# Optimization experiments

Measured on AMD Instinct MI355X. Metric: run time of the kernel, lower is better.

Reference implementation:

```python
import jax, jax.numpy as jnp
import numpy as np

M, N, D = 4096, 50, 100
HID = 512
T_FINAL, S0 = 1.0, 0.0
R = 0.05      # rate in phi(t,X,Y,Z) = R*(Y - sum(X*Z))
SIG = 0.4     # sigma(t,X,Y) = SIG * diag(X)


def _xavier(key, fan_in, fan_out):
    lim = float(np.sqrt(6.0 / (fan_in + fan_out)))
    return jax.random.uniform(key, (fan_in, fan_out), jnp.float32, -lim, lim)


def setup_inputs() -> dict:
    key = jax.random.key(0)
    k_dw, k_xi, k0, k1, k2, k3, k4 = jax.random.split(key, 7)
    dt = (T_FINAL - S0) / N
    # fetch_minibatch(): Dt[:,0]=s, Dt[:,1:]=dt; DW[:,1:]=sqrt(dt)*normal; then cumsum
    Dt = jnp.concatenate([jnp.full((M, 1, 1), S0, jnp.float32),
                          jnp.full((M, N, 1), dt, jnp.float32)], axis=1)
    DW = jnp.concatenate([jnp.zeros((M, 1, D), jnp.float32),
                          jnp.sqrt(dt) * jax.random.normal(k_dw, (M, N, D), jnp.float32)], axis=1)
    t = jnp.cumsum(Dt, axis=1)   # (M, N+1, 1)
    W = jnp.cumsum(DW, axis=1)   # (M, N+1, D)
    Xi = jnp.where(jnp.arange(D) % 2 == 0, 1.0, 0.5)[None, :].astype(jnp.float32)  # (1, D)
    sizes = [D + 1, HID, HID, HID, HID, 1]
    keys = [k0, k1, k2, k3, k4]
    inp = {"t": t, "W": W, "Xi": Xi}
    for i in range(5):
        inp[f"Wm{i}"] = _xavier(keys[i], sizes[i], sizes[i + 1])
        inp[f"b{i}"] = jnp.zeros((sizes[i + 1],), jnp.float32)
    return inp


def _mlp(params, tX):
    # neural_net.forward: sin activations on hidden layers, linear out
    h = tX
    for Wl, bl in params[:-1]:
        h = jnp.sin(h @ Wl + bl)
    Wl, bl = params[-1]
    return h @ Wl + bl  # (M, 1)


def _net_u_Du(params, t, X):
    # u = fn_u([t, X]); Du = d(sum u)/dX via VJP with ones cotangent
    u, vjp = jax.vjp(lambda X_: _mlp(params, jnp.concatenate([t, X_], axis=1)), X)
    (Du,) = vjp(jnp.ones_like(u))
    return u, Du


def _loss(t, W, Xi, params):
    t0, W0 = t[:, 0, :], W[:, 0, :]
    X0 = jnp.tile(Xi, (M, 1))
    Y0, Z0 = _net_u_Du(params, t0, X0)

    def step(carry, inp):
        t0, W0, X0, Y0, Z0, acc = carry
        t1, W1 = inp                                   # (M,1), (M,D)
        dt = t1 - t0
        dW = W1 - W0
        s_dW = SIG * X0 * dW                           # diag(SIG*X0) @ dW, elementwise
        phi = R * (Y0 - jnp.sum(X0 * Z0, axis=1, keepdims=True))
        Y1_tilde = Y0 + phi * dt + jnp.sum(Z0 * s_dW, axis=1, keepdims=True)
        X1 = X0 + s_dW                                 # mu = 0 (Black-Scholes-Barenblatt)
        Y1, Z1 = _net_u_Du(params, t1, X1)
        acc = acc + jnp.sum((Y1 - Y1_tilde) ** 2)
        return (t1, W1, X1, Y1, Z1, acc), None

    ts = jnp.moveaxis(t[:, 1:, :], 1, 0)  # (N, M, 1)
    Ws = jnp.moveaxis(W[:, 1:, :], 1, 0)  # (N, M, D)
    (tN, WN, XN, YN, ZN, sum0N), _ = jax.lax.scan(
        step, (t0, W0, X0, Y0, Z0, jnp.float32(0.0)), (ts, Ws))
    gX = jnp.sum(XN ** 2, axis=1, keepdims=True)       # g(X) = |X|^2
    loss_uT = jnp.sum((YN - gX) ** 2)
    loss_DuT = jnp.sum((ZN - 2.0 * XN) ** 2)
    return (sum0N + loss_uT + loss_DuT) / M            # loss_n == 1 (default)


def reference(t, W, Xi, Wm0, b0, Wm1, b1, Wm2, b2, Wm3, b3, Wm4, b4):
    params = [(Wm0, b0), (Wm1, b1), (Wm2, b2), (Wm3, b3), (Wm4, b4)]
    return _loss(t, W, Xi, params)
```

## Files before the change

kernel.cpp:

```cpp
#include <hip/hip_runtime.h>
#include <cstdint>
#include <cstddef>

#define MM 4096
#define NSTEP 50
#define DD 100
#define HID 512
#define K0P 128
#define SIGC 0.4f
#define RC 0.05f
#define BMR 16
#define NWG (MM / BMR)
#define GSC 16.0f

typedef long fp8x8;
typedef float f32x4 __attribute__((ext_vector_type(4)));
union Pack4 { __bf16 h[4]; uint2 u2; };

typedef const __attribute__((address_space(1))) void* gvp;
typedef __attribute__((address_space(3))) void* lvp;
static __device__ __forceinline__ void load_lds16(const void* g, void* l) {
    __builtin_amdgcn_global_load_lds((gvp)g, (lvp)l, 16, 0, 0);
}

template <int N>
static __device__ __forceinline__ void wait_vmcnt() {
    if constexpr (N == 0)      asm volatile("s_waitcnt vmcnt(0)" ::: "memory");
    else if constexpr (N == 1) asm volatile("s_waitcnt vmcnt(1)" ::: "memory");
    else if constexpr (N == 2) asm volatile("s_waitcnt vmcnt(2)" ::: "memory");
    else if constexpr (N == 4) asm volatile("s_waitcnt vmcnt(4)" ::: "memory");
    __builtin_amdgcn_sched_barrier(0);
}

static __device__ __forceinline__ unsigned char to_fp8(float x) {
    return (unsigned char)(__builtin_amdgcn_cvt_pk_fp8_f32(x, 0.f, 0, false) & 0xff);
}
static __device__ __forceinline__ unsigned pack4_fp8(float a, float b, float c, float d) {
    int w = __builtin_amdgcn_cvt_pk_fp8_f32(a, b, 0, false);
    w = __builtin_amdgcn_cvt_pk_fp8_f32(c, d, w, true);
    return (unsigned)w;
}

__global__ void k_transpose(const float* __restrict__ in, unsigned char* __restrict__ out,
                            int Ksrc, int Kpad, int N) {
    int idx = blockIdx.x * 256 + threadIdx.x;
    if (idx >= N * Kpad) return;
    int n = idx / Kpad, k = idx - n * Kpad;
    out[idx] = (k < Ksrc) ? to_fp8(in[k * N + n]) : (unsigned char)0;
}

__global__ void k_cast(const float* __restrict__ in, unsigned char* __restrict__ out,
                       int Rsrc, int Rpad, int C) {
    int idx = blockIdx.x * 256 + threadIdx.x;
    if (idx >= Rpad * C) return;
    int r = idx / C;
    out[idx] = (r < Rsrc) ? to_fp8(in[idx]) : (unsigned char)0;
}

__global__ __launch_bounds__(256) void k_init(const float* __restrict__ t,
                                              const float* __restrict__ Xi,
                                              float* __restrict__ X0,
                                              unsigned char* __restrict__ tXg) {
    int m = blockIdx.x * 4 + (threadIdx.x >> 6);
    int lane = threadIdx.x & 63;
    for (int ii = 0; ii < 2; ii++) {
        int d = lane + ii * 64;
        if (d < DD) {
            float x = Xi[d];
            X0[m * DD + d] = x;
            tXg[(size_t)m * K0P + 1 + d] = to_fp8(x);
        } else if (d < K0P - 1) {
            tXg[(size_t)m * K0P + 1 + d] = 0;
        }
    }
    if (lane == 0) tXg[(size_t)m * K0P] = to_fp8(t[m * (NSTEP + 1)]);
}

template <int K, int NBLK, int NJB, int ASTR, int EPI>
__device__ __forceinline__ void phaseP(
    int tid, const unsigned char* __restrict__ Bw,
    const char* __restrict__ Rin, char* __restrict__ Rout, char* __restrict__ Bb,
    const float* __restrict__ bias, const float* __restrict__ W4,
    Pack4 (&stash)[2][2], float* __restrict__ u_lds) {

    constexpr int NKB = K / 64;
    constexpr int NJ  = NBLK / 128;
    constexpr int CB  = NBLK * 64;
    constexpr int SB  = CB / 8;
    constexpr int I   = SB / 1024;
    constexpr int NQ  = NJB * NKB;

    const int wave = tid >> 6, lane = tid & 63;
    const int lr = lane & 15, lg = lane >> 4;
    const int am = lr;
    const int wrow0 = wave * (NBLK / 8);

    int bRow[I], bG[I];
    #pragma unroll
    for (int it = 0; it < I; it++) {
        int c16 = it * 64 + lane;
        bRow[it] = c16 >> 2;
        bG[it]   = (c16 & 3) ^ ((bRow[it] >> 1) & 3);
    }

    #define STG(q)                                                              \
        {   char* dst_ = Bb + ((q) % 3) * CB + wave * SB;                       \
            _Pragma("unroll")                                                   \
            for (int it = 0; it < I; it++)                                      \
                load_lds16(Bw + (size_t)(((q) / NKB) * NBLK + wrow0 + bRow[it]) * K \
                               + ((q) % NKB) * 64 + bG[it] * 16,                \
                           dst_ + it * 1024); }

    STG(0)
    if (NQ > 1) STG(1)

    float up = 0.f;
    f32x4 acc[NJ];
    #pragma unroll
    for (int q = 0; q < NQ; q++) {
        const int jb = q / NKB, kb = q % NKB;
        if (kb == 0) {
            #pragma unroll
            for (int nj = 0; nj < NJ; nj++) acc[nj] = f32x4{0.f, 0.f, 0.f, 0.f};
        }
        if (q + 1 < NQ) wait_vmcnt<I>(); else wait_vmcnt<0>();
        if (q + 2 < NQ) STG(q + 2)
        const char* slot = Bb + (q % 3) * CB + wave * SB;
        #pragma unroll
        for (int ks = 0; ks < 2; ks++) {
            int kcA = kb * 8 + ks * 4 + lg;
            fp8x8 aF = *(const fp8x8*)(Rin + am * ASTR +
                        ((((kcA >> 1) ^ (am & 7))) << 4) + (kcA & 1) * 8);
            int kcB = ks * 4 + lg;
            #pragma unroll
            for (int nj = 0; nj < NJ; nj++) {
                int rl = nj * 16 + lr;
                fp8x8 bF = *(const fp8x8*)(slot + rl * 64 +
                            ((((kcB >> 1) ^ ((rl >> 1) & 3))) << 4) + (kcB & 1) * 8);
                acc[nj] = __builtin_amdgcn_mfma_f32_16x16x32_fp8_fp8(
                    bF, aF, acc[nj], 0, 0, 0);
            }
        }
        if (kb == NKB - 1) {
            #pragma unroll
            for (int nj = 0; nj < NJ; nj++) {
                const int n0 = jb * NBLK + wrow0 + nj * 16 + lg * 4;
                if (EPI == 3) {
                    f32x4 z = acc[nj];
                    z *= (1.0f / GSC);
                    *(f32x4*)((float*)Rout + am * 132 + n0) = z;
                } else {
                    const int po = am * 512 + (((n0 >> 4) ^ (am & 7)) << 4) +
                                   ((n0 >> 3) & 1) * 8 + (n0 & 7);
                    if (EPI == 0) {
                        f32x4 bv = *(const f32x4*)(bias + n0);
                        float s[4], c[4];
                        #pragma unroll
                        for (int r = 0; r < 4; r++)
                            __sincosf(acc[nj][r] + bv[r], &s[r], &c[r]);
                        *(unsigned*)(Rout + po) = pack4_fp8(s[0], s[1], s[2], s[3]);
                        Pack4 pc;
                        #pragma unroll
                        for (int r = 0; r < 4; r++) pc.h[r] = (__bf16)c[r];
                        stash[jb][nj] = pc;
                    } else if (EPI == 1) {
                        f32x4 bv = *(const f32x4*)(bias + n0);
                        f32x4 wv = *(const f32x4*)(W4 + n0);
                        float g[4];
                        #pragma unroll
                        for (int r = 0; r < 4; r++) {
                            float s, c;
                            __sincosf(acc[nj][r] + bv[r], &s, &c);
                            up += s * wv[r];
                            g[r] = c * wv[r] * GSC;
                        }
                        *(unsigned*)(Rout + po) = pack4_fp8(g[0], g[1], g[2], g[3]);
                    } else {
                        Pack4 pm = stash[jb][nj];
                        *(unsigned*)(Rout + po) = pack4_fp8(
                            acc[nj][0] * (float)pm.h[0], acc[nj][1] * (float)pm.h[1],
                            acc[nj][2] * (float)pm.h[2], acc[nj][3] * (float)pm.h[3]);
                    }
                }
            }
        }
    }
    #undef STG

    if (EPI == 1) {
        up += __shfl_xor(up, 16);
        up += __shfl_xor(up, 32);
        if (lg == 0) atomicAdd(&u_lds[am], up);
    }
}

__global__ __launch_bounds__(512, 1) void mega(
    const float* __restrict__ t, const float* __restrict__ W,
    const unsigned char* __restrict__ wt0, const unsigned char* __restrict__ wt1,
    const unsigned char* __restrict__ wt2, const unsigned char* __restrict__ wt3,
    const unsigned char* __restrict__ wd0, const unsigned char* __restrict__ wd1,
    const unsigned char* __restrict__ wd2, const unsigned char* __restrict__ wd3,
    const float* __restrict__ b0, const float* __restrict__ b1,
    const float* __restrict__ b2, const float* __restrict__ b3,
    const float* __restrict__ W4, const float* __restrict__ b4,
    unsigned char* __restrict__ tXg, float* __restrict__ X,
    float* __restrict__ Ytil, float* __restrict__ accG, int n) {

    extern __shared__ char lds[];
    char*  tXL   = lds;
    char*  R0    = lds + 2048;
    char*  R1    = lds + 10240;
    float* Zf    = (float*)(lds + 18432);
    char*  Bb    = lds + 27648;
    float* u_lds = (float*)(lds + 76800);

    const int tid = threadIdx.x;
    const int wgrow = blockIdx.x * BMR;
    const int em = tid >> 5, edg = tid & 31, ed0 = edg * 4;
    const int grow = wgrow + em;
    const int lane = tid & 63, wave = tid >> 6;
    const float b4v = b4[0];

    Pack4 st0[2][2], st1[2][2], st2[2][2];

    if (tid < 128) {
        int m = tid >> 3, pc = tid & 7;
        load_lds16(tXg + (size_t)(wgrow + m) * K0P + ((pc ^ (m & 7)) << 4),
                   tXL + wave * 1024 + lane * 16);
    }
    __syncthreads();

    phaseP<128, 256, 2, 128, 0>(tid, wt0, tXL, R0, Bb, b0, nullptr, st0, u_lds);
    __syncthreads();
    phaseP<512, 256, 2, 512, 0>(tid, wt1, R0, R1, Bb, b1, nullptr, st1, u_lds);
    __syncthreads();
    phaseP<512, 256, 2, 512, 0>(tid, wt2, R1, R0, Bb, b2, nullptr, st2, u_lds);
    __syncthreads();
    if (tid < BMR) u_lds[tid] = 0.f;
    __syncthreads();
    phaseP<512, 256, 2, 512, 1>(tid, wt3, R0, R1, Bb, b3, W4, st0 , u_lds);
    __syncthreads();
    phaseP<512, 256, 2, 512, 2>(tid, wd3, R1, R0, Bb, nullptr, nullptr, st2, u_lds);
    __syncthreads();
    phaseP<512, 256, 2, 512, 2>(tid, wd2, R0, R1, Bb, nullptr, nullptr, st1, u_lds);
    __syncthreads();
    phaseP<512, 256, 2, 512, 2>(tid, wd1, R1, R0, Bb, nullptr, nullptr, st0, u_lds);
    __syncthreads();
    phaseP<512, 128, 1, 512, 3>(tid, wd0, R0, (char*)Zf, Bb, nullptr, nullptr, st0, u_lds);
    __syncthreads();

    float u_reg = u_lds[em] + b4v;
    float resid_l = 0.f;
    if (n >= 1 && edg == 0) {
        float dd = u_reg - Ytil[grow];
        resid_l = dd * dd;
    }
    const float* Zs = Zf + em * 132;
    if (n < NSTEP) {
        float t0v = t[grow * (NSTEP + 1) + n];
        float t1v = t[grow * (NSTEP + 1) + n + 1];
        const float* Wr = W + ((size_t)grow * (NSTEP + 1) + n) * DD;
        float pXZ = 0.f, pZs = 0.f;
        #pragma unroll
        for (int i = 0; i < 4; i++) {
            int d = ed0 + i;
            if (d < DD) {
                float x0 = X[grow * DD + d];
                float z = Zs[1 + d];
                float dWv = Wr[DD + d] - Wr[d];
                float s = SIGC * x0 * dWv;
                pXZ += x0 * z;
                pZs += z * s;
                float x1 = x0 + s;
                X[grow * DD + d] = x1;
                tXg[(size_t)grow * K0P + 1 + d] = to_fp8(x1);
            }
        }
        pXZ += __shfl_xor(pXZ, 1); pXZ += __shfl_xor(pXZ, 2);
        pXZ += __shfl_xor(pXZ, 4); pXZ += __shfl_xor(pXZ, 8);
        pXZ += __shfl_xor(pXZ, 16);
        pZs += __shfl_xor(pZs, 1); pZs += __shfl_xor(pZs, 2);
        pZs += __shfl_xor(pZs, 4); pZs += __shfl_xor(pZs, 8);
        pZs += __shfl_xor(pZs, 16);
        if (edg == 0) {
            float phi = RC * (u_reg - pXZ);
            Ytil[grow] = u_reg + phi * (t1v - t0v) + pZs;
            tXg[(size_t)grow * K0P] = to_fp8(t1v);
        }
    } else {
        float gX = 0.f, sD = 0.f;
        #pragma unroll
        for (int i = 0; i < 4; i++) {
            int d = ed0 + i;
            if (d < DD) {
                float x0 = X[grow * DD + d];
                float z = Zs[1 + d];
                gX += x0 * x0;
                float e = z - 2.f * x0;
                sD += e * e;
            }
        }
        gX += __shfl_xor(gX, 1); gX += __shfl_xor(gX, 2);
        gX += __shfl_xor(gX, 4); gX += __shfl_xor(gX, 8);
        gX += __shfl_xor(gX, 16);
        sD += __shfl_xor(sD, 1); sD += __shfl_xor(sD, 2);
        sD += __shfl_xor(sD, 4); sD += __shfl_xor(sD, 8);
        sD += __shfl_xor(sD, 16);
        if (edg == 0) {
            float e = u_reg - gX;
            resid_l += e * e + sD;
        }
    }

    float r = resid_l;
    r += __shfl_xor(r, 32);
    r += __shfl_xor(r, 16);
    r += __shfl_xor(r, 8);
    r += __shfl_xor(r, 4);
    r += __shfl_xor(r, 2);
    r += __shfl_xor(r, 1);
    float* red = u_lds + 16;
    if (lane == 0) red[wave] = r;
    __syncthreads();
    if (tid == 0) {
        float s = 0.f;
        #pragma unroll
        for (int i = 0; i < 8; i++) s += red[i];
        atomicAdd(accG, s);
    }
}

__global__ void k_final(const float* __restrict__ acc, float* __restrict__ out) {
    out[0] = acc[0] / (float)MM;
}

extern "C" void kernel_launch(void* const* d_in, const int* in_sizes, int n_in,
                              void* d_out, int out_size, void* d_ws, size_t ws_size,
                              hipStream_t stream) {
    (void)in_sizes; (void)n_in; (void)out_size; (void)ws_size;
    const float* t  = (const float*)d_in[0];
    const float* W  = (const float*)d_in[1];
    const float* Xi = (const float*)d_in[2];
    const float* Wm[5];
    const float* bb[5];
    for (int i = 0; i < 5; i++) {
        Wm[i] = (const float*)d_in[3 + 2 * i];
        bb[i] = (const float*)d_in[4 + 2 * i];
    }

    char* p = (char*)d_ws;
    auto alloc = [&](size_t bytes) -> void* {
        void* r = (void*)p;
        p += (bytes + 255) & ~(size_t)255;
        return r;
    };

    unsigned char* wt[4];
    wt[0] = (unsigned char*)alloc((size_t)HID * K0P);
    for (int i = 1; i < 4; i++) wt[i] = (unsigned char*)alloc((size_t)HID * HID);
    unsigned char* wd[4];
    wd[0] = (unsigned char*)alloc((size_t)K0P * HID);
    for (int i = 1; i < 4; i++) wd[i] = (unsigned char*)alloc((size_t)HID * HID);
    unsigned char* tXg = (unsigned char*)alloc((size_t)MM * K0P);
    float* X    = (float*)alloc((size_t)MM * DD * 4);
    float* Ytil = (float*)alloc((size_t)MM * 4);
    float* acc  = (float*)alloc(256);

    hipMemsetAsync(acc, 0, 256, stream);

    k_transpose<<<(HID * K0P + 255) / 256, 256, 0, stream>>>(Wm[0], wt[0], 101, K0P, HID);
    for (int i = 1; i < 4; i++)
        k_transpose<<<(HID * HID + 255) / 256, 256, 0, stream>>>(Wm[i], wt[i], HID, HID, HID);
    k_cast<<<(K0P * HID + 255) / 256, 256, 0, stream>>>(Wm[0], wd[0], 101, K0P, HID);
    for (int i = 1; i < 4; i++)
        k_cast<<<(HID * HID + 255) / 256, 256, 0, stream>>>(Wm[i], wd[i], HID, HID, HID);

    k_init<<<MM / 4, 256, 0, stream>>>(t, Xi, X, tXg);

    const int LDSB = 77056;
    hipFuncSetAttribute((const void*)mega,
                        hipFuncAttributeMaxDynamicSharedMemorySize, LDSB);

    for (int n = 0; n <= NSTEP; n++) {
        mega<<<dim3(NWG), dim3(512), LDSB, stream>>>(
            t, W,
            wt[0], wt[1], wt[2], wt[3],
            wd[0], wd[1], wd[2], wd[3],
            bb[0], bb[1], bb[2], bb[3],
            Wm[4], bb[4],
            tXg, X, Ytil, acc, n);
    }

    k_final<<<1, 1, 0, stream>>>(acc, (float*)d_out);
}
```

Baseline: 1.469 ms.

## Fuse three timesteps per kernel launch and widen GEMM N-block to 512

The mega kernel now runs SPAN=3 consecutive timesteps in one launch. X and Ytil stay in registers across those steps, and the fp8 network input is rewritten directly into LDS instead of being reloaded from global memory each step. This cuts the launch count about threefold and removes per-step global round-trips for X and the input tile. The GEMM phases also drop the two-pass N loop: each wave now covers 512 output columns with four accumulators, which roughly doubles the B staging buffers to about 125 KB of LDS and adds register pressure.

```diff
diff --git a/kernel.cpp b/kernel.cpp
--- a/kernel.cpp
+++ b/kernel.cpp
@@ -12,6 +12,7 @@
 #define BMR 16
 #define NWG (MM / BMR)
 #define GSC 16.0f
+#define SPAN 3
 
 typedef long fp8x8;
 typedef float f32x4 __attribute__((ext_vector_type(4)));
@@ -76,19 +77,18 @@
     if (lane == 0) tXg[(size_t)m * K0P] = to_fp8(t[m * (NSTEP + 1)]);
 }
 
-template <int K, int NBLK, int NJB, int ASTR, int EPI>
+template <int K, int NBLK, int ASTR, int EPI>
 __device__ __forceinline__ void phaseP(
     int tid, const unsigned char* __restrict__ Bw,
     const char* __restrict__ Rin, char* __restrict__ Rout, char* __restrict__ Bb,
     const float* __restrict__ bias, const float* __restrict__ W4,
-    Pack4 (&stash)[2][2], float* __restrict__ u_lds) {
-
-    constexpr int NKB = K / 64;
+    Pack4 (&stash)[4], float* __restrict__ u_lds) {
+
+    constexpr int NQ  = K / 64;
     constexpr int NJ  = NBLK / 128;
     constexpr int CB  = NBLK * 64;
     constexpr int SB  = CB / 8;
     constexpr int I   = SB / 1024;
-    constexpr int NQ  = NJB * NKB;
 
     const int wave = tid >> 6, lane = tid & 63;
     const int lr = lane & 15, lg = lane >> 4;
@@ -107,28 +107,23 @@
         {   char* dst_ = Bb + ((q) % 3) * CB + wave * SB;                       \
             _Pragma("unroll")                                                   \
             for (int it = 0; it < I; it++)                                      \
-                load_lds16(Bw + (size_t)(((q) / NKB) * NBLK + wrow0 + bRow[it]) * K \
-                               + ((q) % NKB) * 64 + bG[it] * 16,                \
+                load_lds16(Bw + (size_t)(wrow0 + bRow[it]) * K                  \
+                               + (q) * 64 + bG[it] * 16,                        \
                            dst_ + it * 1024); }
 
     STG(0)
     if (NQ > 1) STG(1)
 
     float up = 0.f;
-    f32x4 acc[NJ];
+    f32x4 acc[NJ] = {};
     #pragma unroll
     for (int q = 0; q < NQ; q++) {
-        const int jb = q / NKB, kb = q % NKB;
-        if (kb == 0) {
-            #pragma unroll
-            for (int nj = 0; nj < NJ; nj++) acc[nj] = f32x4{0.f, 0.f, 0.f, 0.f};
-        }
         if (q + 1 < NQ) wait_vmcnt<I>(); else wait_vmcnt<0>();
         if (q + 2 < NQ) STG(q + 2)
         const char* slot = Bb + (q % 3) * CB + wave * SB;
         #pragma unroll
         for (int ks = 0; ks < 2; ks++) {
-            int kcA = kb * 8 + ks * 4 + lg;
+            int kcA = q * 8 + ks * 4 + lg;
             fp8x8 aF = *(const fp8x8*)(Rin + am * ASTR +
                         ((((kcA >> 1) ^ (am & 7))) << 4) + (kcA & 1) * 8);
             int kcB = ks * 4 + lg;
@@ -141,51 +136,50 @@
                     bF, aF, acc[nj], 0, 0, 0);
             }
         }
-        if (kb == NKB - 1) {
-            #pragma unroll
-            for (int nj = 0; nj < NJ; nj++) {
-                const int n0 = jb * NBLK + wrow0 + nj * 16 + lg * 4;
-                if (EPI == 3) {
-                    f32x4 z = acc[nj];
-                    z *= (1.0f / GSC);
-                    *(f32x4*)((float*)Rout + am * 132 + n0) = z;
-                } else {
-                    const int po = am * 512 + (((n0 >> 4) ^ (am & 7)) << 4) +
-                                   ((n0 >> 3) & 1) * 8 + (n0 & 7);
-                    if (EPI == 0) {
-                        f32x4 bv = *(const f32x4*)(bias + n0);
-                        float s[4], c[4];
-                        #pragma unroll
-                        for (int r = 0; r < 4; r++)
-                            __sincosf(acc[nj][r] + bv[r], &s[r], &c[r]);
-                        *(unsigned*)(Rout + po) = pack4_fp8(s[0], s[1], s[2], s[3]);
-                        Pack4 pc;
-                        #pragma unroll
-                        for (int r = 0; r < 4; r++) pc.h[r] = (__bf16)c[r];
-                        stash[jb][nj] = pc;
-                    } else if (EPI == 1) {
-                        f32x4 bv = *(const f32x4*)(bias + n0);
-                        f32x4 wv = *(const f32x4*)(W4 + n0);
-                        float g[4];
-                        #pragma unroll
-                        for (int r = 0; r < 4; r++) {
-                            float s, c;
-                            __sincosf(acc[nj][r] + bv[r], &s, &c);
-                            up += s * wv[r];
-                            g[r] = c * wv[r] * GSC;
-                        }
-                        *(unsigned*)(Rout + po) = pack4_fp8(g[0], g[1], g[2], g[3]);
-                    } else {
-                        Pack4 pm = stash[jb][nj];
-                        *(unsigned*)(Rout + po) = pack4_fp8(
-                            acc[nj][0] * (float)pm.h[0], acc[nj][1] * (float)pm.h[1],
-                            acc[nj][2] * (float)pm.h[2], acc[nj][3] * (float)pm.h[3]);
-                    }
+    }
+    #undef STG
+
+    #pragma unroll
+    for (int nj = 0; nj < NJ; nj++) {
+        const int n0 = wrow0 + nj * 16 + lg * 4;
+        if (EPI == 3) {
+            f32x4 z = acc[nj];
+            z *= (1.0f / GSC);
+            *(f32x4*)((float*)Rout + am * 132 + n0) = z;
+        } else {
+            const int po = am * 512 + (((n0 >> 4) ^ (am & 7)) << 4) +
+                           ((n0 >> 3) & 1) * 8 + (n0 & 7);
+            if (EPI == 0) {
+                f32x4 bv = *(const f32x4*)(bias + n0);
+                float s[4], c[4];
+                #pragma unroll
+                for (int r = 0; r < 4; r++)
+                    __sincosf(acc[nj][r] + bv[r], &s[r], &c[r]);
+                *(unsigned*)(Rout + po) = pack4_fp8(s[0], s[1], s[2], s[3]);
+                Pack4 pc;
+                #pragma unroll
+                for (int r = 0; r < 4; r++) pc.h[r] = (__bf16)c[r];
+                stash[nj] = pc;
+            } else if (EPI == 1) {
+                f32x4 bv = *(const f32x4*)(bias + n0);
+                f32x4 wv = *(const f32x4*)(W4 + n0);
+                float g[4];
+                #pragma unroll
+                for (int r = 0; r < 4; r++) {
+                    float s, c;
+                    __sincosf(acc[nj][r] + bv[r], &s, &c);
+                    up += s * wv[r];
+                    g[r] = c * wv[r] * GSC;
                 }
+                *(unsigned*)(Rout + po) = pack4_fp8(g[0], g[1], g[2], g[3]);
+            } else {
+                Pack4 pm = stash[nj];
+                *(unsigned*)(Rout + po) = pack4_fp8(
+                    acc[nj][0] * (float)pm.h[0], acc[nj][1] * (float)pm.h[1],
+                    acc[nj][2] * (float)pm.h[2], acc[nj][3] * (float)pm.h[3]);
             }
         }
     }
-    #undef STG
 
     if (EPI == 1) {
         up += __shfl_xor(up, 16);
@@ -204,15 +198,15 @@
     const float* __restrict__ b2, const float* __restrict__ b3,
     const float* __restrict__ W4, const float* __restrict__ b4,
     unsigned char* __restrict__ tXg, float* __restrict__ X,
-    float* __restrict__ Ytil, float* __restrict__ accG, int n) {
+    float* __restrict__ Ytil, float* __restrict__ accG, int n0) {
 
     extern __shared__ char lds[];
     char*  tXL   = lds;
     char*  R0    = lds + 2048;
     char*  R1    = lds + 10240;
     float* Zf    = (float*)(lds + 18432);
-    char*  Bb    = lds + 27648;
-    float* u_lds = (float*)(lds + 76800);
+    char*  Bb    = lds + 26880;
+    float* u_lds = (float*)(lds + 125184);
 
     const int tid = threadIdx.x;
     const int wgrow = blockIdx.x * BMR;
@@ -221,7 +215,16 @@
     const int lane = tid & 63, wave = tid >> 6;
     const float b4v = b4[0];
 
-    Pack4 st0[2][2], st1[2][2], st2[2][2];
+    Pack4 st0[4], st1[4], st2[4];
+
+    float x[4];
+    #pragma unroll
+    for (int i = 0; i < 4; i++) {
+        int d = ed0 + i;
+        x[i] = (d < DD) ? X[grow * DD + d] : 0.f;
+    }
+    float ytil = Ytil[grow];
+    float resid_l = 0.f;
 
     if (tid < 128) {
         int m = tid >> 3, pc = tid & 7;
@@ -230,87 +233,100 @@
     }
     __syncthreads();
 
-    phaseP<128, 256, 2, 128, 0>(tid, wt0, tXL, R0, Bb, b0, nullptr, st0, u_lds);
-    __syncthreads();
-    phaseP<512, 256, 2, 512, 0>(tid, wt1, R0, R1, Bb, b1, nullptr, st1, u_lds);
-    __syncthreads();
-    phaseP<512, 256, 2, 512, 0>(tid, wt2, R1, R0, Bb, b2, nullptr, st2, u_lds);
-    __syncthreads();
-    if (tid < BMR) u_lds[tid] = 0.f;
-    __syncthreads();
-    phaseP<512, 256, 2, 512, 1>(tid, wt3, R0, R1, Bb, b3, W4, st0 , u_lds);
-    __syncthreads();
-    phaseP<512, 256, 2, 512, 2>(tid, wd3, R1, R0, Bb, nullptr, nullptr, st2, u_lds);
-    __syncthreads();
-    phaseP<512, 256, 2, 512, 2>(tid, wd2, R0, R1, Bb, nullptr, nullptr, st1, u_lds);
-    __syncthreads();
-    phaseP<512, 256, 2, 512, 2>(tid, wd1, R1, R0, Bb, nullptr, nullptr, st0, u_lds);
-    __syncthreads();
-    phaseP<512, 128, 1, 512, 3>(tid, wd0, R0, (char*)Zf, Bb, nullptr, nullptr, st0, u_lds);
-    __syncthreads();
-
-    float u_reg = u_lds[em] + b4v;
-    float resid_l = 0.f;
-    if (n >= 1 && edg == 0) {
-        float dd = u_reg - Ytil[grow];
-        resid_l = dd * dd;
-    }
-    const float* Zs = Zf + em * 132;
-    if (n < NSTEP) {
-        float t0v = t[grow * (NSTEP + 1) + n];
-        float t1v = t[grow * (NSTEP + 1) + n + 1];
-        const float* Wr = W + ((size_t)grow * (NSTEP + 1) + n) * DD;
-        float pXZ = 0.f, pZs = 0.f;
-        #pragma unroll
-        for (int i = 0; i < 4; i++) {
-            int d = ed0 + i;
-            if (d < DD) {
-                float x0 = X[grow * DD + d];
-                float z = Zs[1 + d];
-                float dWv = Wr[DD + d] - Wr[d];
-                float s = SIGC * x0 * dWv;
-                pXZ += x0 * z;
-                pZs += z * s;
-                float x1 = x0 + s;
-                X[grow * DD + d] = x1;
-                tXg[(size_t)grow * K0P + 1 + d] = to_fp8(x1);
-            }
+    for (int s = 0; s < SPAN; s++) {
+        const int n = n0 + s;
+
+        phaseP<128, 512, 128, 0>(tid, wt0, tXL, R0, Bb, b0, nullptr, st0, u_lds);
+        __syncthreads();
+        phaseP<512, 512, 512, 0>(tid, wt1, R0, R1, Bb, b1, nullptr, st1, u_lds);
+        __syncthreads();
+        phaseP<512, 512, 512, 0>(tid, wt2, R1, R0, Bb, b2, nullptr, st2, u_lds);
+        __syncthreads();
+        if (tid < BMR) u_lds[tid] = 0.f;
+        __syncthreads();
+        phaseP<512, 512, 512, 1>(tid, wt3, R0, R1, Bb, b3, W4, st0 , u_lds);
+        __syncthreads();
+        phaseP<512, 512, 512, 2>(tid, wd3, R1, R0, Bb, nullptr, nullptr, st2, u_lds);
+        __syncthreads();
+        phaseP<512, 512, 512, 2>(tid, wd2, R0, R1, Bb, nullptr, nullptr, st1, u_lds);
+        __syncthreads();
+        phaseP<512, 512, 512, 2>(tid, wd1, R1, R0, Bb, nullptr, nullptr, st0, u_lds);
+        __syncthreads();
+        phaseP<512, 128, 512, 3>(tid, wd0, R0, (char*)Zf, Bb, nullptr, nullptr, st0, u_lds);
+        __syncthreads();
+
+        float u_reg = u_lds[em] + b4v;
+        if (n >= 1 && edg == 0) {
+            float dd = u_reg - ytil;
+            resid_l += dd * dd;
         }
-        pXZ += __shfl_xor(pXZ, 1); pXZ += __shfl_xor(pXZ, 2);
-        pXZ += __shfl_xor(pXZ, 4); pXZ += __shfl_xor(pXZ, 8);
-        pXZ += __shfl_xor(pXZ, 16);
-        pZs += __shfl_xor(pZs, 1); pZs += __shfl_xor(pZs, 2);
-        pZs += __shfl_xor(pZs, 4); pZs += __shfl_xor(pZs, 8);
-        pZs += __shfl_xor(pZs, 16);
-        if (edg == 0) {
-            float phi = RC * (u_reg - pXZ);
-            Ytil[grow] = u_reg + phi * (t1v - t0v) + pZs;
-            tXg[(size_t)grow * K0P] = to_fp8(t1v);
+        const float* Zs = Zf + em * 132;
+        if (n < NSTEP) {
+            float t0v = t[grow * (NSTEP + 1) + n];
+            float t1v = t[grow * (NSTEP + 1) + n + 1];
+            const float* Wr = W + ((size_t)grow * (NSTEP + 1) + n) * DD;
+            float pXZ = 0.f, pZs = 0.f;
+            #pragma unroll
+            for (int i = 0; i < 4; i++) {
+                int d = ed0 + i;
+                if (d < DD) {
+                    float z = Zs[1 + d];
+                    float dWv = Wr[DD + d] - Wr[d];
+                    float sdw = SIGC * x[i] * dWv;
+                    pXZ += x[i] * z;
+                    pZs += z * sdw;
+                    x[i] += sdw;
+                    unsigned char v8 = to_fp8(x[i]);
+                    int c = 1 + d;
+                    tXL[em * 128 + (((c >> 4) ^ (em & 7)) << 4) + (c & 15)] = v8;
+                    tXg[(size_t)grow * K0P + c] = v8;
+                }
+            }
+            pXZ += __shfl_xor(pXZ, 1); pXZ += __shfl_xor(pXZ, 2);
+            pXZ += __shfl_xor(pXZ, 4); pXZ += __shfl_xor(pXZ, 8);
+            pXZ += __shfl_xor(pXZ, 16);
+            pZs += __shfl_xor(pZs, 1); pZs += __shfl_xor(pZs, 2);
+            pZs += __shfl_xor(pZs, 4); pZs += __shfl_xor(pZs, 8);
+            pZs += __shfl_xor(pZs, 16);
+            if (edg == 0) {
+                float phi = RC * (u_reg - pXZ);
+                ytil = u_reg + phi * (t1v - t0v) + pZs;
+                unsigned char t8 = to_fp8(t1v);
+                tXL[em * 128 + ((em & 7) << 4)] = t8;
+                tXg[(size_t)grow * K0P] = t8;
+            }
+        } else {
+            float gX = 0.f, sD = 0.f;
+            #pragma unroll
+            for (int i = 0; i < 4; i++) {
+                int d = ed0 + i;
+                if (d < DD) {
+                    float z = Zs[1 + d];
+                    gX += x[i] * x[i];
+                    float e = z - 2.f * x[i];
+                    sD += e * e;
+                }
+            }
+            gX += __shfl_xor(gX, 1); gX += __shfl_xor(gX, 2);
+            gX += __shfl_xor(gX, 4); gX += __shfl_xor(gX, 8);
+            gX += __shfl_xor(gX, 16);
+            sD += __shfl_xor(sD, 1); sD += __shfl_xor(sD, 2);
+            sD += __shfl_xor(sD, 4); sD += __shfl_xor(sD, 8);
+            sD += __shfl_xor(sD, 16);
+            if (edg == 0) {
+                float e = u_reg - gX;
+                resid_l += e * e + sD;
+            }
         }
-    } else {
-        float gX = 0.f, sD = 0.f;
-        #pragma unroll
-        for (int i = 0; i < 4; i++) {
-            int d = ed0 + i;
-            if (d < DD) {
-                float x0 = X[grow * DD + d];
-                float z = Zs[1 + d];
-                gX += x0 * x0;
-                float e = z - 2.f * x0;
-                sD += e * e;
-            }
-        }
-        gX += __shfl_xor(gX, 1); gX += __shfl_xor(gX, 2);
-        gX += __shfl_xor(gX, 4); gX += __shfl_xor(gX, 8);
-        gX += __shfl_xor(gX, 16);
-        sD += __shfl_xor(sD, 1); sD += __shfl_xor(sD, 2);
-        sD += __shfl_xor(sD, 4); sD += __shfl_xor(sD, 8);
-        sD += __shfl_xor(sD, 16);
-        if (edg == 0) {
-            float e = u_reg - gX;
-            resid_l += e * e + sD;
-        }
-    }
+        __syncthreads();
+    }
+
+    #pragma unroll
+    for (int i = 0; i < 4; i++) {
+        int d = ed0 + i;
+        if (d < DD) X[grow * DD + d] = x[i];
+    }
+    if (edg == 0) Ytil[grow] = ytil;
 
     float r = resid_l;
     r += __shfl_xor(r, 32);
@@ -377,18 +393,18 @@
 
     k_init<<<MM / 4, 256, 0, stream>>>(t, Xi, X, tXg);
 
-    const int LDSB = 77056;
+    const int LDSB = 125440;
     hipFuncSetAttribute((const void*)mega,
                         hipFuncAttributeMaxDynamicSharedMemorySize, LDSB);
 
-    for (int n = 0; n <= NSTEP; n++) {
+    for (int n0 = 0; n0 <= NSTEP; n0 += SPAN) {
         mega<<<dim3(NWG), dim3(512), LDSB, stream>>>(
             t, W,
             wt[0], wt[1], wt[2], wt[3],
             wd[0], wd[1], wd[2], wd[3],
             bb[0], bb[1], bb[2], bb[3],
             Wm[4], bb[4],
-            tXg, X, Ytil, acc, n);
+            tXg, X, Ytil, acc, n0);
     }
 
     k_final<<<1, 1, 0, stream>>>(acc, (float*)d_out);
```

Result: slower. 5.561 ms (+278.5%).
